# Kernel optimization log

Hardware: AMD Instinct MI355X
Metric: run time of the kernel (lower is better)

The kernel has to match this reference:

```python
import jax, jax.numpy as jnp
import numpy as np
import math

B, T, D, SLOTS, TOPK = 8, 4096, 512, 128, 8


def setup_inputs() -> dict:
    key = jax.random.key(0)
    kq, kK, kV = jax.random.split(key, 3)
    # xavier_uniform for [slots, d_model]: bound = sqrt(6/(slots+d_model))
    bound = math.sqrt(6.0 / (SLOTS + D))
    return {
        "q": jax.random.normal(kq, (B, T, D), dtype=jnp.float32),
        "K": jax.random.uniform(kK, (SLOTS, D), minval=-bound, maxval=bound, dtype=jnp.float32),
        "V": jax.random.uniform(kV, (SLOTS, D), minval=-bound, maxval=bound, dtype=jnp.float32),
        "salience": jnp.zeros((SLOTS,), dtype=jnp.float32),
        "topk": TOPK,
    }


def reference(q, K, V, salience, topk):
    # q: [B,T,D], K/V: [S,D], salience: [S]
    Bq, Tq, Dq = q.shape
    k = min(topk, K.shape[0])
    scores = jnp.einsum('btd,sd->bts', q, K) / jnp.sqrt(jnp.float32(Dq))
    scores = scores + salience[None, None, :]
    topk_scores, topk_indices = jax.lax.top_k(scores, k)          # [B,T,k]
    attention_weights = jax.nn.softmax(topk_scores, axis=-1)      # [B,T,k]
    V_selected = V[topk_indices]                                  # [B,T,k,D] gather
    read_vectors = jnp.einsum('btk,btkd->btd', attention_weights, V_selected)
    return read_vectors, attention_weights
```

## Files before the change

kernel.cpp:

```cpp
#include <hip/hip_runtime.h>
#include <hip/hip_bf16.h>
#include <math.h>

#define R_TOTAL 32768
#define DM      512
#define NSLOT   128
#define KSEL    8

typedef _Float16 half8 __attribute__((ext_vector_type(8)));
typedef float    floatx4 __attribute__((ext_vector_type(4)));

__global__ void smb_splitK(const float* __restrict__ Km,
                           _Float16* __restrict__ K1, _Float16* __restrict__ K2) {
  const int i = blockIdx.x * 256 + threadIdx.x;
  const float f = Km[i] * 256.0f;
  const _Float16 h = (_Float16)f;
  K1[i] = h;
  K2[i] = (_Float16)(f - (float)h);
}

__device__ __forceinline__ void load16_lds(const _Float16* g, _Float16* l) {
  __builtin_amdgcn_global_load_lds(
      (const __attribute__((address_space(1))) unsigned int*)g,
      (__attribute__((address_space(3))) unsigned int*)l, 16, 0, 0);
}

__global__ __launch_bounds__(512, 4) void smb_main(
    const float* __restrict__ q,
    const _Float16* __restrict__ K1,
    const _Float16* __restrict__ K2,
    const float* __restrict__ Vm,
    const float* __restrict__ sal,
    float* __restrict__ outv,
    float* __restrict__ outw)
{
  __shared__ _Float16 stage[2][8][NSLOT][8];
  __shared__ float slab[64][132];

  const int t  = threadIdx.x;
  const int w  = t >> 6;
  const int l  = t & 63;
  const int li = l & 15;
  const int kg = l >> 4;
  const int rg = w >> 1;
  const int sh = w & 1;
  const int r0b = blockIdx.x * 64;
  const int r0w = r0b + rg * 16;

  const float* qrow = q + (size_t)(r0w + li) * DM + kg * 8;

  floatx4 acc[4];
#pragma unroll
  for (int g = 0; g < 4; ++g) acc[g] = (floatx4){0.f, 0.f, 0.f, 0.f};

#pragma unroll
  for (int p = 0; p < 2; ++p) {
    const _Float16* src = (w < 4 ? K1 : K2) + (size_t)(p * 64 + l) * DM + (w & 3) * 8;
    load16_lds(src, &stage[0][w][p * 64][0]);
  }
  float4 q0c = *(const float4*)(qrow + 0);
  float4 q1c = *(const float4*)(qrow + 4);
  __syncthreads();

#pragma unroll 2
  for (int c = 0; c < 16; ++c) {
    const int cb = c & 1, nb = cb ^ 1;
    float4 q0n, q1n;
    if (c < 15) {
#pragma unroll
      for (int p = 0; p < 2; ++p) {
        const _Float16* src = (w < 4 ? K1 : K2)
                            + (size_t)(p * 64 + l) * DM + (c + 1) * 32 + (w & 3) * 8;
        load16_lds(src, &stage[nb][w][p * 64][0]);
      }
      q0n = *(const float4*)(qrow + (c + 1) * 32);
      q1n = *(const float4*)(qrow + (c + 1) * 32 + 4);
    }

    half8 a1, a2;
#pragma unroll
    for (int j = 0; j < 4; ++j) {
      const float f0 = q0c[j] * 16.0f;
      const float f1 = q1c[j] * 16.0f;
      const _Float16 h0 = (_Float16)f0;
      const _Float16 h1 = (_Float16)f1;
      a1[j]     = h0;  a2[j]     = (_Float16)(f0 - (float)h0);
      a1[4 + j] = h1;  a2[4 + j] = (_Float16)(f1 - (float)h1);
    }
#pragma unroll
    for (int g = 0; g < 4; ++g) {
      const int slot = sh * 64 + g * 16 + li;
      const half8 b1 = *(const half8*)&stage[cb][kg][slot][0];
      const half8 b2 = *(const half8*)&stage[cb][4 + kg][slot][0];
      acc[g] = __builtin_amdgcn_mfma_f32_16x16x32_f16(a1, b1, acc[g], 0, 0, 0);
      acc[g] = __builtin_amdgcn_mfma_f32_16x16x32_f16(a2, b1, acc[g], 0, 0, 0);
      acc[g] = __builtin_amdgcn_mfma_f32_16x16x32_f16(a1, b2, acc[g], 0, 0, 0);
    }
    q0c = q0n; q1c = q1n;
    __syncthreads();
  }

  const float den = sqrtf((float)DM);
#pragma unroll
  for (int g = 0; g < 4; ++g) {
    const int col = sh * 64 + g * 16 + li;
    const float sv = sal[col];
#pragma unroll
    for (int i = 0; i < 4; ++i) {
      const float s = (acc[g][i] * 0.000244140625f) / den + sv;
      slab[rg * 16 + kg * 4 + i][col] = s;
    }
  }
  __syncthreads();

  const int row = t >> 3;
  const int lq  = t & 7;

  float bs[8]; int bi[8];
#pragma unroll
  for (int p = 0; p < 8; ++p) { bs[p] = -3.0e38f; bi[p] = 0x7fffffff; }

#pragma unroll
  for (int jj = 0; jj < 16; ++jj) {
    const int   j = jj * 8 + lq;
    const float s = slab[row][j];
    bool c[8];
#pragma unroll
    for (int p = 0; p < 8; ++p) c[p] = s > bs[p];
    float nb[8]; int ni[8];
    nb[0] = c[0] ? s : bs[0];
    ni[0] = c[0] ? j : bi[0];
#pragma unroll
    for (int p = 7; p >= 1; --p) {
      nb[p] = c[p] ? (c[p - 1] ? bs[p - 1] : s) : bs[p];
      ni[p] = c[p] ? (c[p - 1] ? bi[p - 1] : j) : bi[p];
    }
#pragma unroll
    for (int p = 0; p < 8; ++p) { bs[p] = nb[p]; bi[p] = ni[p]; }
  }

  float ts[8]; int ti_[8];
#pragma unroll
  for (int r = 0; r < 8; ++r) {
    float hs = bs[0]; int hi = bi[0];
#pragma unroll
    for (int m = 1; m <= 4; m <<= 1) {
      const float os = __shfl_xor(hs, m, 64);
      const int   oi = __shfl_xor(hi, m, 64);
      if (os > hs || (os == hs && oi < hi)) { hs = os; hi = oi; }
    }
    ts[r] = hs; ti_[r] = hi;
    if (bs[0] == hs && bi[0] == hi) {
#pragma unroll
      for (int p = 0; p < 7; ++p) { bs[p] = bs[p + 1]; bi[p] = bi[p + 1]; }
      bs[7] = -3.0e38f; bi[7] = 0x7fffffff;
    }
  }

  float tw[8];
  const float mx = ts[0];
  float esum = 0.0f;
#pragma unroll
  for (int r = 0; r < 8; ++r) { tw[r] = expf(ts[r] - mx); esum += tw[r]; }
#pragma unroll
  for (int r = 0; r < 8; ++r) tw[r] /= esum;

  if (lq == 0) {
#pragma unroll
    for (int r = 0; r < 8; ++r) outw[(size_t)(r0b + row) * KSEL + r] = tw[r];
  }

  const float4* __restrict__ V4 = (const float4*)Vm;
  float4* __restrict__ O4 = (float4*)outv;
  const size_t obase = (size_t)(r0b + row) * (DM / 4);
#pragma unroll 4
  for (int cc = 0; cc < 16; ++cc) {
    const int cdx = cc * 8 + lq;
    float4 a; a.x = a.y = a.z = a.w = 0.0f;
#pragma unroll
    for (int r = 0; r < 8; ++r) {
      const float4 v = V4[(size_t)ti_[r] * (DM / 4) + cdx];
      a.x = fmaf(tw[r], v.x, a.x);
      a.y = fmaf(tw[r], v.y, a.y);
      a.z = fmaf(tw[r], v.z, a.z);
      a.w = fmaf(tw[r], v.w, a.w);
    }
    O4[obase + cdx] = a;
  }
}

extern "C" void kernel_launch(void* const* d_in, const int* in_sizes, int n_in,
                              void* d_out, int out_size, void* d_ws, size_t ws_size,
                              hipStream_t stream) {
  const float* q   = (const float*)d_in[0];
  const float* Km  = (const float*)d_in[1];
  const float* Vm  = (const float*)d_in[2];
  const float* sal = (const float*)d_in[3];

  float* outv = (float*)d_out;
  float* outw = outv + (size_t)R_TOTAL * DM;

  _Float16* K1 = (_Float16*)d_ws;
  _Float16* K2 = K1 + (size_t)NSLOT * DM;

  hipLaunchKernelGGL(smb_splitK, dim3((NSLOT * DM) / 256), dim3(256), 0, stream, Km, K1, K2);
  hipLaunchKernelGGL(smb_main, dim3(R_TOTAL / 64), dim3(512), 0, stream,
                     q, K1, K2, Vm, sal, outv, outw);
}
```

Measured before the change: 67.67 us.

## Pre-tile split K into stage layout and prefetch q two chunks ahead

The K preprocessing kernel now writes the hi and lo fp16 halves into one buffer, already ordered as [chunk][group][slot][8]. Each wave's global-to-LDS load is then a contiguous 1 KB run instead of 16-byte pieces spread across rows 1 KB apart. The main loop also loads q two chunks ahead instead of one, to hide more global latency. The costs are extra live registers for the deeper q prefetch and scattered stores in the small prep kernel.

```diff
diff --git a/kernel.cpp b/kernel.cpp
--- a/kernel.cpp
+++ b/kernel.cpp
@@ -10,13 +10,18 @@
 typedef _Float16 half8 __attribute__((ext_vector_type(8)));
 typedef float    floatx4 __attribute__((ext_vector_type(4)));
 
-__global__ void smb_splitK(const float* __restrict__ Km,
-                           _Float16* __restrict__ K1, _Float16* __restrict__ K2) {
+__global__ void smb_prepK(const float* __restrict__ Km, _Float16* __restrict__ Ks) {
   const int i = blockIdx.x * 256 + threadIdx.x;
-  const float f = Km[i] * 256.0f;
-  const _Float16 h = (_Float16)f;
-  K1[i] = h;
-  K2[i] = (_Float16)(f - (float)h);
+  const int slot = i >> 9;
+  const int d    = i & 511;
+  const float f  = Km[i] * 256.0f;
+  const _Float16 h  = (_Float16)f;
+  const _Float16 lo = (_Float16)(f - (float)h);
+  const int c  = d >> 5;
+  const int kg = (d >> 3) & 3;
+  const int j  = d & 7;
+  Ks[((((c * 8) + kg    ) * NSLOT + slot) << 3) + j] = h;
+  Ks[((((c * 8) + 4 + kg) * NSLOT + slot) << 3) + j] = lo;
 }
 
 __device__ __forceinline__ void load16_lds(const _Float16* g, _Float16* l) {
@@ -27,8 +32,7 @@
 
 __global__ __launch_bounds__(512, 4) void smb_main(
     const float* __restrict__ q,
-    const _Float16* __restrict__ K1,
-    const _Float16* __restrict__ K2,
+    const _Float16* __restrict__ Ks,
     const float* __restrict__ Vm,
     const float* __restrict__ sal,
     float* __restrict__ outv,
@@ -55,26 +59,29 @@
 
 #pragma unroll
   for (int p = 0; p < 2; ++p) {
-    const _Float16* src = (w < 4 ? K1 : K2) + (size_t)(p * 64 + l) * DM + (w & 3) * 8;
-    load16_lds(src, &stage[0][w][p * 64][0]);
+    const _Float16* src = Ks + ((((size_t)0 * 8 + w) * NSLOT + p * 64 + l) << 3);
+    load16_lds(src, &stage[0][w][p * 64 + l][0]);
   }
   float4 q0c = *(const float4*)(qrow + 0);
   float4 q1c = *(const float4*)(qrow + 4);
+  float4 q0n = *(const float4*)(qrow + 32);
+  float4 q1n = *(const float4*)(qrow + 36);
   __syncthreads();
 
 #pragma unroll 2
   for (int c = 0; c < 16; ++c) {
     const int cb = c & 1, nb = cb ^ 1;
-    float4 q0n, q1n;
+    float4 q0nn, q1nn;
     if (c < 15) {
 #pragma unroll
       for (int p = 0; p < 2; ++p) {
-        const _Float16* src = (w < 4 ? K1 : K2)
-                            + (size_t)(p * 64 + l) * DM + (c + 1) * 32 + (w & 3) * 8;
-        load16_lds(src, &stage[nb][w][p * 64][0]);
+        const _Float16* src = Ks + ((((size_t)(c + 1) * 8 + w) * NSLOT + p * 64 + l) << 3);
+        load16_lds(src, &stage[nb][w][p * 64 + l][0]);
       }
-      q0n = *(const float4*)(qrow + (c + 1) * 32);
-      q1n = *(const float4*)(qrow + (c + 1) * 32 + 4);
+    }
+    if (c < 14) {
+      q0nn = *(const float4*)(qrow + (c + 2) * 32);
+      q1nn = *(const float4*)(qrow + (c + 2) * 32 + 4);
     }
 
     half8 a1, a2;
@@ -97,6 +104,7 @@
       acc[g] = __builtin_amdgcn_mfma_f32_16x16x32_f16(a1, b2, acc[g], 0, 0, 0);
     }
     q0c = q0n; q1c = q1n;
+    if (c < 14) { q0n = q0nn; q1n = q1nn; }
     __syncthreads();
   }
 
@@ -200,10 +208,9 @@
   float* outv = (float*)d_out;
   float* outw = outv + (size_t)R_TOTAL * DM;
 
-  _Float16* K1 = (_Float16*)d_ws;
-  _Float16* K2 = K1 + (size_t)NSLOT * DM;
-
-  hipLaunchKernelGGL(smb_splitK, dim3((NSLOT * DM) / 256), dim3(256), 0, stream, Km, K1, K2);
+  _Float16* Ks = (_Float16*)d_ws;
+
+  hipLaunchKernelGGL(smb_prepK, dim3((NSLOT * DM) / 256), dim3(256), 0, stream, Km, Ks);
   hipLaunchKernelGGL(smb_main, dim3(R_TOTAL / 64), dim3(512), 0, stream,
-                     q, K1, K2, Vm, sal, outv, outw);
-}
+                     q, Ks, Vm, sal, outv, outw);
+}
```

Result: faster. 56.81 us (-16.1%).
